# Kernel tuning notes

Hardware: AMD Instinct MI355X
Metric: run time of the kernel (lower is better)

Reference implementation:

```python
import jax, jax.numpy as jnp
import numpy as np

N, C, L, K = 8, 128, 1024, 100   # batch, channels, encoded seq len, num_negatives
TEMP = 0.5                        # contrastive temperature
EPS = 1e-8                        # cosine-similarity norm clamp (torch default)


def setup_inputs() -> dict:
    key = jax.random.key(0)
    kz, kc, kn = jax.random.split(key, 3)
    z = jax.random.normal(kz, (N, C, L), dtype=jnp.float32)
    c = jax.random.normal(kc, (N, C, L + 1), dtype=jnp.float32)
    # Uniform sampling of K distinct indices per (n, l), excluding l itself:
    # equivalent to torch.multinomial(ones(L,L)-eye(L), K) per row, per sample.
    noise = jax.random.uniform(kn, (N, L, L), dtype=jnp.float32)
    noise = noise - 2.0 * jnp.eye(L, dtype=jnp.float32)  # push self-index below everything
    _, neg_inds = jax.lax.top_k(noise, K)                # (N, L, K) int32, distinct, != l
    return {"z": z, "c": c, "neg_inds": neg_inds.astype(jnp.int32)}


def reference(z, c, neg_inds):
    # z: (N, C, L) unmasked convencoder features; c: (N, C, L+1) transformer out
    n, ch, l = z.shape
    z_seq = jnp.transpose(z, (0, 2, 1))                  # (N, L, C)
    # gather negatives: (N, L, K, C)
    negatives = z_seq[jnp.arange(n)[:, None, None], neg_inds]
    # drop start token, move to (N, L, 1, C)
    c_seq = jnp.transpose(c[..., 1:], (0, 2, 1))[:, :, None, :]
    z_tgt = z_seq[:, :, None, :]                         # (N, L, 1, C)
    targets = jnp.concatenate([z_tgt, negatives], axis=2)  # (N, L, K+1, C)
    # cosine similarity along C with torch-style eps clamping
    dot = jnp.sum(c_seq * targets, axis=-1)              # (N, L, K+1)
    c_norm = jnp.maximum(jnp.sqrt(jnp.sum(c_seq * c_seq, axis=-1)), EPS)
    t_norm = jnp.maximum(jnp.sqrt(jnp.sum(targets * targets, axis=-1)), EPS)
    logits = dot / (c_norm * t_norm) / TEMP              # (N, L, K+1)
    # mask negatives that exactly equal the context vector
    neg_in_tgt = jnp.all(c_seq == negatives, axis=-1)    # (N, L, K)
    neg_logits = jnp.where(neg_in_tgt, -jnp.inf, logits[:, :, 1:])
    logits = jnp.concatenate([logits[:, :, :1], neg_logits], axis=2)
    return logits.reshape(-1, K + 1)                     # (N*L, K+1)
```

## Files before the change

kernel.cpp:

```cpp
#include <hip/hip_runtime.h>
#include <math.h>

#define N 8
#define C 128
#define L 1024
#define K 100
#define TEMP 0.5f
#define EPS 1e-8f
#define NT (N * L)
#define ROWS 32

typedef _Float16 half8 __attribute__((ext_vector_type(8)));
typedef float f32x4 __attribute__((ext_vector_type(4)));


__global__ void __launch_bounds__(512)
transpose_frag(const float* __restrict__ z, const float* __restrict__ c,
               half8* __restrict__ zf, half8* __restrict__ cf,
               float* __restrict__ zp, float* __restrict__ cp) {
    __shared__ float tile[64][65];
    __shared__ float part[8][64];
    const int which = blockIdx.z >> 3;
    const int n = blockIdx.z & 7;
    const float* src = which ? c : z;
    half8* dst = which ? cf : zf;
    float* pdst = which ? cp : zp;
    const int slen = which ? (L + 1) : L;
    const int off = which;
    const int l0 = blockIdx.x * 64;
    const int c0 = blockIdx.y * 64;
    const int tx = threadIdx.x;
    const int ty = threadIdx.y;
#pragma unroll
    for (int i = 0; i < 8; i++) {
        int chn = c0 + ty + i * 8;
        tile[ty + i * 8][tx] = src[((size_t)(n * C + chn)) * slen + off + l0 + tx];
    }
    __syncthreads();
    float p = 0.f;
    half8 hv;
#pragma unroll
    for (int q = 0; q < 8; q++) {
        float v = tile[ty * 8 + q][tx];
        p += v * v;
        hv[q] = (_Float16)v;
    }
    const int l = l0 + tx;
    const int ch = c0 + ty * 8;
    const int ks = ch >> 5, kg = (ch >> 3) & 3;
    dst[(((size_t)(n * 64 + (l >> 4)) * 4 + ks) << 6) + (l & 15) + (kg << 4)] = hv;
    part[ty][tx] = p;
    __syncthreads();
    if (ty == 0) {
        float sm = 0.f;
#pragma unroll
        for (int i = 0; i < 8; i++) sm += part[i][tx];
        pdst[(((size_t)n << 10) + l0 + tx) * 2 + (c0 >> 6)] = sm;
    }
}

__global__ void __launch_bounds__(512, 2)
gemm_gather(const half8* __restrict__ zf, const half8* __restrict__ cf,
            const int* __restrict__ neg_inds,
            const float* __restrict__ zp, const float* __restrict__ cp,
            const float* __restrict__ z_orig, const float* __restrict__ c_orig,
            float* __restrict__ out) {
    __shared__ _Float16 dotH[ROWS * L];
    __shared__ float2 zpl[L];
    const int tid  = threadIdx.x;
    const int lane = tid & 63;
    const int w    = tid >> 6;
    const int n    = blockIdx.x >> 5;
    const int tA   = blockIdx.x & 31;

    const float2* zp2 = (const float2*)zp + ((size_t)n << 10);
    for (int i = tid; i < L; i += 512) zpl[i] = zp2[i];

    const size_t nbase = (size_t)n << 14;
    half8 a[2][4];
#pragma unroll
    for (int at = 0; at < 2; at++)
#pragma unroll
        for (int ks = 0; ks < 4; ks++)
            a[at][ks] = cf[nbase + ((((tA << 1) + at) * 4 + ks) << 6) + lane];

    f32x4 acc[2][8];
#pragma unroll
    for (int at = 0; at < 2; at++)
#pragma unroll
        for (int i = 0; i < 8; i++)
#pragma unroll
            for (int r = 0; r < 4; r++) acc[at][i][r] = 0.f;

#pragma unroll
    for (int ks = 0; ks < 4; ks++) {
        half8 b[8];
#pragma unroll
        for (int nt = 0; nt < 8; nt++)
            b[nt] = zf[nbase + ((size_t)(((w << 3) + nt) * 4 + ks) << 6) + lane];
#pragma unroll
        for (int nt = 0; nt < 8; nt++)
            acc[0][nt] = __builtin_amdgcn_mfma_f32_16x16x32_f16(a[0][ks], b[nt], acc[0][nt], 0, 0, 0);
#pragma unroll
        for (int nt = 0; nt < 8; nt++)
            acc[1][nt] = __builtin_amdgcn_mfma_f32_16x16x32_f16(a[1][ks], b[nt], acc[1][nt], 0, 0, 0);
    }

    const int r16 = lane & 15;
    const int kg  = lane >> 4;
#pragma unroll
    for (int at = 0; at < 2; at++)
#pragma unroll
        for (int nt = 0; nt < 8; nt++)
#pragma unroll
            for (int r = 0; r < 4; r++)
                dotH[((at << 4) + (kg << 2) + r) * L + (w << 7) + (nt << 4) + r16]
                    = (_Float16)acc[at][nt][r];
    __syncthreads();

    const int row = tid >> 4;
    const int sub = tid & 15;
    const int t   = (tA << 5) + row;
    const int ntg = (n << 10) + t;
    const float2 cpv = ((const float2*)cp)[ntg];
    const float cn = cpv.x + cpv.y;
    const float rs_c = 2.0f * rsqrtf(fmaxf(cn, EPS * EPS));
    const int* ni = neg_inds + (size_t)ntg * K;
    float* orow = out + (size_t)ntg * (K + 1);

    for (int kk = sub; kk <= K; kk += 16) {
        const int col = (kk == 0) ? t : ni[kk - 1];
        const float dot = (float)dotH[row * L + col];
        const float2 tv = zpl[col];
        const float tn = tv.x + tv.y;
        float logit = dot * rs_c * rsqrtf(fmaxf(tn, EPS * EPS));
        if (kk > 0) {
            const float ds = cn - 2.f * dot + tn;
            if (ds < 0.05f * cn) {
                bool eq = true;
                for (int q = 0; q < C; q++) {
                    float cv = c_orig[((size_t)(n * C + q)) * (L + 1) + t + 1];
                    float zv = z_orig[((size_t)(n * C + q)) * L + col];
                    eq = eq && (cv == zv);
                }
                if (eq) logit = -INFINITY;
            }
        }
        orow[kk] = logit;
    }
}

extern "C" void kernel_launch(void* const* d_in, const int* in_sizes, int n_in,
                              void* d_out, int out_size, void* d_ws, size_t ws_size,
                              hipStream_t stream) {
    const float* z   = (const float*)d_in[0];
    const float* c   = (const float*)d_in[1];
    const int*   neg = (const int*)d_in[2];
    float* out = (float*)d_out;

    half8* zf = (half8*)d_ws;
    half8* cf = zf + (size_t)N * 16384;
    float* zp = (float*)(cf + (size_t)N * 16384);
    float* cp = zp + (size_t)NT * 2;

    transpose_frag<<<dim3(L / 64, C / 64, 16), dim3(64, 8), 0, stream>>>(z, c, zf, cf, zp, cp);
    gemm_gather<<<dim3(N * (L / ROWS)), 512, 0, stream>>>(zf, cf, neg, zp, cp, z, c, out);
}
```

Before: 76.28 us.

## Stage neg indices and outputs in LDS, swizzle dot tile, precompute norms

Loads the block's negative indices into shared memory with coalesced reads and stages the output logits in shared memory, then writes them back as one contiguous coalesced stream. The per-column reciprocal target norms are computed once per column instead of once per gathered element, and the fp16 dot tile is XOR-swizzled by row group to reduce LDS bank conflicts on store. Each thread now handles 7 consecutive logits instead of a strided set. This adds about 30 KB more LDS per block, which may limit the two-blocks-per-CU occupancy target.

```diff
diff --git a/kernel.cpp b/kernel.cpp
--- a/kernel.cpp
+++ b/kernel.cpp
@@ -66,15 +66,26 @@
             const float* __restrict__ z_orig, const float* __restrict__ c_orig,
             float* __restrict__ out) {
     __shared__ _Float16 dotH[ROWS * L];
-    __shared__ float2 zpl[L];
+    __shared__ float ztn[L];
+    __shared__ float ztr[L];
+    __shared__ int   nil[ROWS * K];
+    __shared__ float outF[ROWS * (K + 1)];
     const int tid  = threadIdx.x;
     const int lane = tid & 63;
     const int w    = tid >> 6;
     const int n    = blockIdx.x >> 5;
     const int tA   = blockIdx.x & 31;
+    const int ntg0 = (n << 10) + (tA << 5);
 
     const float2* zp2 = (const float2*)zp + ((size_t)n << 10);
-    for (int i = tid; i < L; i += 512) zpl[i] = zp2[i];
+    for (int i = tid; i < L; i += 512) {
+        float2 tv = zp2[i];
+        float tn = tv.x + tv.y;
+        ztn[i] = tn;
+        ztr[i] = rsqrtf(fmaxf(tn, EPS * EPS));
+    }
+    const int* nb = neg_inds + (size_t)ntg0 * K;
+    for (int i = tid; i < ROWS * K; i += 512) nil[i] = nb[i];
 
     const size_t nbase = (size_t)n << 14;
     half8 a[2][4];
@@ -113,41 +124,48 @@
 #pragma unroll
         for (int nt = 0; nt < 8; nt++)
 #pragma unroll
-            for (int r = 0; r < 4; r++)
-                dotH[((at << 4) + (kg << 2) + r) * L + (w << 7) + (nt << 4) + r16]
-                    = (_Float16)acc[at][nt][r];
+            for (int r = 0; r < 4; r++) {
+                const int row = (at << 4) + (kg << 2) + r;
+                const int col = (w << 7) + (nt << 4) + r16;
+                dotH[row * L + (col ^ (kg << 4))] = (_Float16)acc[at][nt][r];
+            }
     __syncthreads();
 
     const int row = tid >> 4;
     const int sub = tid & 15;
     const int t   = (tA << 5) + row;
-    const int ntg = (n << 10) + t;
-    const float2 cpv = ((const float2*)cp)[ntg];
+    const int ksw = ((row >> 2) & 3) << 4;
+    const float2 cpv = ((const float2*)cp)[ntg0 + row];
     const float cn = cpv.x + cpv.y;
     const float rs_c = 2.0f * rsqrtf(fmaxf(cn, EPS * EPS));
-    const int* ni = neg_inds + (size_t)ntg * K;
-    float* orow = out + (size_t)ntg * (K + 1);
 
-    for (int kk = sub; kk <= K; kk += 16) {
-        const int col = (kk == 0) ? t : ni[kk - 1];
-        const float dot = (float)dotH[row * L + col];
-        const float2 tv = zpl[col];
-        const float tn = tv.x + tv.y;
-        float logit = dot * rs_c * rsqrtf(fmaxf(tn, EPS * EPS));
-        if (kk > 0) {
-            const float ds = cn - 2.f * dot + tn;
-            if (ds < 0.05f * cn) {
-                bool eq = true;
-                for (int q = 0; q < C; q++) {
-                    float cv = c_orig[((size_t)(n * C + q)) * (L + 1) + t + 1];
-                    float zv = z_orig[((size_t)(n * C + q)) * L + col];
-                    eq = eq && (cv == zv);
+#pragma unroll
+    for (int j = 0; j < 7; j++) {
+        const int kk = sub * 7 + j;
+        if (kk <= K) {
+            const int col = (kk == 0) ? t : nil[row * K + kk - 1];
+            const float dot = (float)dotH[row * L + (col ^ ksw)];
+            const float tn = ztn[col];
+            float logit = dot * rs_c * ztr[col];
+            if (kk > 0) {
+                const float ds = cn - 2.f * dot + tn;
+                if (ds < 0.05f * cn) {
+                    bool eq = true;
+                    for (int q = 0; q < C; q++) {
+                        float cv = c_orig[((size_t)(n * C + q)) * (L + 1) + t + 1];
+                        float zv = z_orig[((size_t)(n * C + q)) * L + col];
+                        eq = eq && (cv == zv);
+                    }
+                    if (eq) logit = -INFINITY;
                 }
-                if (eq) logit = -INFINITY;
             }
+            outF[row * (K + 1) + kk] = logit;
         }
-        orow[kk] = logit;
     }
+    __syncthreads();
+
+    float* ob = out + (size_t)ntg0 * (K + 1);
+    for (int i = tid; i < ROWS * (K + 1); i += 512) ob[i] = outF[i];
 }
 
 extern "C" void kernel_launch(void* const* d_in, const int* in_sizes, int n_in,
```

Result: faster. 74.68 us (-2.1%).
